# Optimization experiments

Measured on AMD Instinct MI355X. Metric: run time of the kernel, lower is better.

Reference implementation:

```python
import jax, jax.numpy as jnp
import numpy as np

EPS = 1e-6

def setup_inputs() -> dict:
    key = jax.random.key(0)
    S, U, D = 512, 32, 512
    dvecs = jax.random.normal(key, (S, U, D), dtype=jnp.float32)
    w = jnp.array([10.0], dtype=jnp.float32)
    b = jnp.array([-5.0], dtype=jnp.float32)
    return {"dvecs": dvecs, "w": w, "b": b}


def _ge2e_loss(dvecs, w, b):
    S, U, D = dvecs.shape
    # Full centroids [S, D]
    centroids = dvecs.mean(axis=1)
    # Leave-one-out centroids [S, U, D] (equivalent to the roll/unfold/mean trick)
    loo = (dvecs.sum(axis=1, keepdims=True) - dvecs) / (U - 1)
    # Norms, clamped like F.cosine_similarity eps
    dn = jnp.linalg.norm(dvecs, axis=-1)        # [S, U]
    cn = jnp.linalg.norm(centroids, axis=-1)    # [S]
    ln = jnp.linalg.norm(loo, axis=-1)          # [S, U]
    # Cosine sim of every utterance vs every speaker centroid: [S, U, S]
    sim_all = jnp.einsum('sud,jd->suj', dvecs, centroids) / jnp.maximum(dn[..., None] * cn[None, None, :], EPS)
    # Self-speaker column uses the leave-one-out centroid (index_copy in torch code)
    sim_self = jnp.einsum('sud,sud->su', dvecs, loo) / jnp.maximum(dn * ln, EPS)
    spk = jnp.arange(S)
    self_mask = spk[:, None, None] == spk[None, None, :]          # [S, 1, S] -> broadcasts to [S, U, S]
    sim = jnp.where(self_mask, sim_self[..., None], sim_all)
    logits = sim * w[0] + b[0]
    losses = -jax.nn.log_softmax(logits, axis=2)                  # [S, U, S]
    # Select losses[s, u, s] and sum (index_select of diagonal entries)
    return jnp.sum(jnp.where(self_mask, losses, 0.0))


def reference(dvecs, w, b):
    return _ge2e_loss(dvecs, w, b)
```

## Files before the change

### kernel.cpp

```cpp
#include <hip/hip_runtime.h>
#include <math.h>

#define NS 512
#define NU 32
#define ND 512
#define GEPS 1e-6f

typedef float f4 __attribute__((ext_vector_type(4)));
typedef _Float16 half8 __attribute__((ext_vector_type(8)));


__global__ __launch_bounds__(256) void prep_kernel(const float* __restrict__ dvecs,
                                                   _Float16* __restrict__ bpk,
                                                   float* __restrict__ cn2) {
    const int s = blockIdx.x, t = threadIdx.x;
    const float* base = dvecs + (size_t)s * NU * ND;
    const int d0 = t * 2;
    float sx = 0.f, sy = 0.f;
    for (int u = 0; u < NU; ++u) {
        float2 v = *(const float2*)(base + u * ND + d0);
        sx += v.x; sy += v.y;
    }
    sx *= (1.0f / NU); sy *= (1.0f / NU);

    float c2 = sx * sx + sy * sy;
    #pragma unroll
    for (int m = 1; m < 64; m <<= 1) c2 += __shfl_xor(c2, m);
    __shared__ float red[4];
    if ((t & 63) == 0) red[t >> 6] = c2;
    __syncthreads();
    if (t == 0) cn2[s] = red[0] + red[1] + red[2] + red[3];

    _Float16 hx = (_Float16)sx, hy = (_Float16)sy;
    _Float16 lx = (_Float16)(sx - (float)hx), ly = (_Float16)(sy - (float)hy);
    const int ct_g = s >> 4, l15 = s & 15;
    const int tt = d0 >> 5, lg = (d0 >> 3) & 3, j = d0 & 7;
    size_t hbase = ((size_t)(ct_g * 16 + tt)) * 1024 + (lg * 16 + l15) * 8 + j;
    unsigned hi2 = (unsigned)__builtin_bit_cast(unsigned short, hx)
                 | ((unsigned)__builtin_bit_cast(unsigned short, hy) << 16);
    unsigned lo2 = (unsigned)__builtin_bit_cast(unsigned short, lx)
                 | ((unsigned)__builtin_bit_cast(unsigned short, ly) << 16);
    *(unsigned*)(bpk + hbase)       = hi2;
    *(unsigned*)(bpk + hbase + 512) = lo2;
}

__global__ __launch_bounds__(512, 4) void ge2e_mfma(const float* __restrict__ dvecs,
                                                    const _Float16* __restrict__ bpk,
                                                    const float* __restrict__ cn2,
                                                    const float* __restrict__ wp,
                                                    const float* __restrict__ bp,
                                                    float* __restrict__ out) {
    const int s = blockIdx.x, tid = threadIdx.x;
    const int l = tid & 63, wv = tid >> 6;
    const int l15 = l & 15, lg = l >> 4;

    f4 acc[2][4];
    #pragma unroll
    for (int rt = 0; rt < 2; ++rt)
        #pragma unroll
        for (int ct = 0; ct < 4; ++ct) acc[rt][ct] = (f4){0.f, 0.f, 0.f, 0.f};
    float dnp[2] = {0.f, 0.f};

    const float*    Ab0 = dvecs + (size_t)s * NU * ND + (size_t)l15 * ND + lg * 8;
    const _Float16* Bb  = bpk + (size_t)(wv * 4) * 16 * 1024 + l * 8;

    for (int t = 0; t < 16; ++t) {
        half8 bh[4], bl[4];
        #pragma unroll
        for (int ct = 0; ct < 4; ++ct) {
            const _Float16* p = Bb + (size_t)(ct * 16 + t) * 1024;
            bh[ct] = *(const half8*)p;
            bl[ct] = *(const half8*)(p + 512);
        }
        half8 ah[2], al[2];
        #pragma unroll
        for (int rt = 0; rt < 2; ++rt) {
            const float* ap = Ab0 + rt * 16 * ND + t * 32;
            f4 a0 = *(const f4*)ap, a1 = *(const f4*)(ap + 4);
            dnp[rt] += a0[0]*a0[0] + a0[1]*a0[1] + a0[2]*a0[2] + a0[3]*a0[3]
                     + a1[0]*a1[0] + a1[1]*a1[1] + a1[2]*a1[2] + a1[3]*a1[3];
            #pragma unroll
            for (int i = 0; i < 4; ++i) {
                _Float16 h0 = (_Float16)a0[i];
                ah[rt][i]     = h0; al[rt][i]     = (_Float16)(a0[i] - (float)h0);
                _Float16 h1 = (_Float16)a1[i];
                ah[rt][4 + i] = h1; al[rt][4 + i] = (_Float16)(a1[i] - (float)h1);
            }
        }
        #pragma unroll
        for (int ct = 0; ct < 4; ++ct)
            #pragma unroll
            for (int rt = 0; rt < 2; ++rt) {
                acc[rt][ct] = __builtin_amdgcn_mfma_f32_16x16x32_f16(ah[rt], bh[ct], acc[rt][ct], 0, 0, 0);
                acc[rt][ct] = __builtin_amdgcn_mfma_f32_16x16x32_f16(ah[rt], bl[ct], acc[rt][ct], 0, 0, 0);
                acc[rt][ct] = __builtin_amdgcn_mfma_f32_16x16x32_f16(al[rt], bh[ct], acc[rt][ct], 0, 0, 0);
                acc[rt][ct] = __builtin_amdgcn_mfma_f32_16x16x32_f16(al[rt], bl[ct], acc[rt][ct], 0, 0, 0);
            }
    }

    #pragma unroll
    for (int rt = 0; rt < 2; ++rt) {
        dnp[rt] += __shfl_xor(dnp[rt], 16);
        dnp[rt] += __shfl_xor(dnp[rt], 32);
    }
    __shared__ float sDn2[32], sSelf[32], sMax[8][32], sSum[8][32], sRow[32];
    if (wv == 0 && l < 16) { sDn2[l15] = dnp[0]; sDn2[16 + l15] = dnp[1]; }
    __syncthreads();

    const float w = wp[0], bb = bp[0];
    const float cn2s = cn2[s];
    float dv[2][4];
    #pragma unroll
    for (int rt = 0; rt < 2; ++rt)
        #pragma unroll
        for (int r = 0; r < 4; ++r) dv[rt][r] = sDn2[rt * 16 + lg * 4 + r];

    const bool owner = (wv == (s >> 6)) && (l15 == (s & 15));
    const int  ctd   = (s >> 4) & 3;

    float dotc[2][4];
    #pragma unroll
    for (int ct = 0; ct < 4; ++ct)
        if (ct == ctd)
            #pragma unroll
            for (int rt = 0; rt < 2; ++rt)
                #pragma unroll
                for (int r = 0; r < 4; ++r) dotc[rt][r] = acc[rt][ct][r];

    #pragma unroll
    for (int ct = 0; ct < 4; ++ct) {
        const float cv = cn2[wv * 64 + ct * 16 + l15];
        #pragma unroll
        for (int rt = 0; rt < 2; ++rt)
            #pragma unroll
            for (int r = 0; r < 4; ++r)
                acc[rt][ct][r] = w * (acc[rt][ct][r] / fmaxf(sqrtf(dv[rt][r] * cv), GEPS)) + bb;
    }
    if (owner) {
        #pragma unroll
        for (int rt = 0; rt < 2; ++rt)
            #pragma unroll
            for (int r = 0; r < 4; ++r) {
                const float d2  = dv[rt][r];
                const float num = (float)NU * dotc[rt][r] - d2;
                const float X   = (float)(NU * NU) * cn2s - 2.0f * NU * dotc[rt][r] + d2;
                const float den = fmaxf(sqrtf(d2) * sqrtf(X), GEPS * (NU - 1));
                const float ls  = w * (num / den) + bb;
                #pragma unroll
                for (int ct = 0; ct < 4; ++ct)
                    if (ct == ctd) acc[rt][ct][r] = ls;
                sSelf[rt * 16 + lg * 4 + r] = ls;
            }
    }

    #pragma unroll
    for (int rt = 0; rt < 2; ++rt)
        #pragma unroll
        for (int r = 0; r < 4; ++r) {
            float mx = -INFINITY;
            #pragma unroll
            for (int ct = 0; ct < 4; ++ct) mx = fmaxf(mx, acc[rt][ct][r]);
            mx = fmaxf(mx, __shfl_xor(mx, 1)); mx = fmaxf(mx, __shfl_xor(mx, 2));
            mx = fmaxf(mx, __shfl_xor(mx, 4)); mx = fmaxf(mx, __shfl_xor(mx, 8));
            float se = 0.f;
            #pragma unroll
            for (int ct = 0; ct < 4; ++ct) se += expf(acc[rt][ct][r] - mx);
            se += __shfl_xor(se, 1); se += __shfl_xor(se, 2);
            se += __shfl_xor(se, 4); se += __shfl_xor(se, 8);
            if (l15 == 0) {
                sMax[wv][rt * 16 + lg * 4 + r] = mx;
                sSum[wv][rt * 16 + lg * 4 + r] = se;
            }
        }
    __syncthreads();

    if (tid < 32) {
        float M = -INFINITY;
        #pragma unroll
        for (int v = 0; v < 8; ++v) M = fmaxf(M, sMax[v][tid]);
        float S = 0.f;
        #pragma unroll
        for (int v = 0; v < 8; ++v) S += sSum[v][tid] * expf(sMax[v][tid] - M);
        sRow[tid] = logf(S) + M - sSelf[tid];
    }
    __syncthreads();
    if (tid == 0) {
        float tot = 0.f;
        #pragma unroll
        for (int u2 = 0; u2 < 32; ++u2) tot += sRow[u2];
        atomicAdd(out, tot);
    }
}

extern "C" void kernel_launch(void* const* d_in, const int* in_sizes, int n_in,
                              void* d_out, int out_size, void* d_ws, size_t ws_size,
                              hipStream_t stream) {
    const float* dvecs = (const float*)d_in[0];
    const float* w     = (const float*)d_in[1];
    const float* b     = (const float*)d_in[2];
    float* out = (float*)d_out;

    _Float16* bpk = (_Float16*)d_ws;
    float*    cn2 = (float*)(bpk + (size_t)32 * 16 * 1024);

    hipMemsetAsync(d_out, 0, sizeof(float), stream);
    prep_kernel<<<NS, 256, 0, stream>>>(dvecs, bpk, cn2);
    ge2e_mfma<<<NS, 512, 0, stream>>>(dvecs, bpk, cn2, w, b, out);
}
```

Baseline: 136.3 us.

## Precompute split-fp16 packed utterance tiles and norms in prep kernel

The prep kernel now also computes per-utterance squared norms and writes the hi/lo fp16 split of every dvec into an MFMA-ready packed layout. The main kernel then loads these packed half8 fragments directly instead of reading fp32 and converting inside its loop, which was replicated across all 8 waves. The cost is an extra write and read of a 32 MB workspace buffer, plus a fallback path kept for when the workspace is too small.

```diff
diff --git a/kernel.cpp b/kernel.cpp
--- a/kernel.cpp
+++ b/kernel.cpp
@@ -10,9 +10,218 @@
 typedef _Float16 half8 __attribute__((ext_vector_type(8)));
 
 
-__global__ __launch_bounds__(256) void prep_kernel(const float* __restrict__ dvecs,
-                                                   _Float16* __restrict__ bpk,
-                                                   float* __restrict__ cn2) {
+__global__ __launch_bounds__(256) void prep_full(const float* __restrict__ dvecs,
+                                                 _Float16* __restrict__ bpk,
+                                                 float* __restrict__ cn2,
+                                                 float* __restrict__ dn2,
+                                                 _Float16* __restrict__ apk) {
+    const int s = blockIdx.x, t = threadIdx.x;
+    const int l = t & 63, wv = t >> 6, l15 = l & 15, lg = l >> 4;
+    const float* base = dvecs + (size_t)s * NU * ND;
+    __shared__ float red[4];
+
+    const int d0 = t * 2;
+    float sx = 0.f, sy = 0.f;
+    #pragma unroll 4
+    for (int u = 0; u < NU; ++u) {
+        float2 v = *(const float2*)(base + u * ND + d0);
+        sx += v.x; sy += v.y;
+    }
+    sx *= (1.0f / NU); sy *= (1.0f / NU);
+    float c2 = sx * sx + sy * sy;
+    #pragma unroll
+    for (int m = 1; m < 64; m <<= 1) c2 += __shfl_xor(c2, m);
+    if ((t & 63) == 0) red[t >> 6] = c2;
+
+    {
+        _Float16 hx = (_Float16)sx, hy = (_Float16)sy;
+        _Float16 lx = (_Float16)(sx - (float)hx), ly = (_Float16)(sy - (float)hy);
+        const int ct_g = s >> 4, cl15 = s & 15;
+        const int tt = d0 >> 5, blg = (d0 >> 3) & 3, j = d0 & 7;
+        size_t hbase = ((size_t)(ct_g * 16 + tt)) * 1024 + (blg * 16 + cl15) * 8 + j;
+        unsigned hi2 = (unsigned)__builtin_bit_cast(unsigned short, hx)
+                     | ((unsigned)__builtin_bit_cast(unsigned short, hy) << 16);
+        unsigned lo2 = (unsigned)__builtin_bit_cast(unsigned short, lx)
+                     | ((unsigned)__builtin_bit_cast(unsigned short, ly) << 16);
+        *(unsigned*)(bpk + hbase)       = hi2;
+        *(unsigned*)(bpk + hbase + 512) = lo2;
+    }
+    __syncthreads();
+    if (t == 0) cn2[s] = red[0] + red[1] + red[2] + red[3];
+
+    {
+        const int u = t >> 3, jj = t & 7;
+        const float* up = base + u * ND + jj * 4;
+        float q = 0.f;
+        #pragma unroll
+        for (int i = 0; i < 16; ++i) {
+            f4 v = *(const f4*)(up + i * 32);
+            q += v[0]*v[0] + v[1]*v[1] + v[2]*v[2] + v[3]*v[3];
+        }
+        q += __shfl_xor(q, 1); q += __shfl_xor(q, 2); q += __shfl_xor(q, 4);
+        if (jj == 0) dn2[s * NU + u] = q;
+    }
+
+    #pragma unroll
+    for (int i = 0; i < 8; ++i) {
+        const int idx = wv * 8 + i;
+        const int rt = idx >> 4, tk = idx & 15;
+        const int u = rt * 16 + l15, k = tk * 32 + lg * 8;
+        const float* ap = base + (size_t)u * ND + k;
+        f4 a0 = *(const f4*)ap;
+        f4 a1 = *(const f4*)(ap + 4);
+        half8 h, lo;
+        #pragma unroll
+        for (int i2 = 0; i2 < 4; ++i2) {
+            _Float16 h0 = (_Float16)a0[i2];
+            h[i2]     = h0; lo[i2]     = (_Float16)(a0[i2] - (float)h0);
+            _Float16 h1 = (_Float16)a1[i2];
+            h[4 + i2] = h1; lo[4 + i2] = (_Float16)(a1[i2] - (float)h1);
+        }
+        _Float16* cb = apk + ((size_t)(s * 2 + rt) * 16 + tk) * 1024 + l * 8;
+        *(half8*)cb         = h;
+        *(half8*)(cb + 512) = lo;
+    }
+}
+
+__global__ __launch_bounds__(512, 4) void ge2e_full(const _Float16* __restrict__ apk,
+                                                    const _Float16* __restrict__ bpk,
+                                                    const float* __restrict__ cn2,
+                                                    const float* __restrict__ dn2,
+                                                    const float* __restrict__ wp,
+                                                    const float* __restrict__ bp,
+                                                    float* __restrict__ out) {
+    const int s = blockIdx.x, tid = threadIdx.x;
+    const int l = tid & 63, wv = tid >> 6;
+    const int l15 = l & 15, lg = l >> 4;
+
+    f4 acc[2][4];
+    #pragma unroll
+    for (int rt = 0; rt < 2; ++rt)
+        #pragma unroll
+        for (int ct = 0; ct < 4; ++ct) acc[rt][ct] = (f4){0.f, 0.f, 0.f, 0.f};
+
+    const _Float16* Ab = apk + (size_t)s * 32 * 1024 + l * 8;
+    const _Float16* Bb = bpk + (size_t)(wv * 4) * 16 * 1024 + l * 8;
+
+    for (int t = 0; t < 16; ++t) {
+        half8 bh[4], bl[4], ah[2], al[2];
+        #pragma unroll
+        for (int ct = 0; ct < 4; ++ct) {
+            const _Float16* p = Bb + (size_t)(ct * 16 + t) * 1024;
+            bh[ct] = *(const half8*)p;
+            bl[ct] = *(const half8*)(p + 512);
+        }
+        #pragma unroll
+        for (int rt = 0; rt < 2; ++rt) {
+            const _Float16* p = Ab + (size_t)(rt * 16 + t) * 1024;
+            ah[rt] = *(const half8*)p;
+            al[rt] = *(const half8*)(p + 512);
+        }
+        #pragma unroll
+        for (int ct = 0; ct < 4; ++ct)
+            #pragma unroll
+            for (int rt = 0; rt < 2; ++rt) {
+                acc[rt][ct] = __builtin_amdgcn_mfma_f32_16x16x32_f16(ah[rt], bh[ct], acc[rt][ct], 0, 0, 0);
+                acc[rt][ct] = __builtin_amdgcn_mfma_f32_16x16x32_f16(ah[rt], bl[ct], acc[rt][ct], 0, 0, 0);
+                acc[rt][ct] = __builtin_amdgcn_mfma_f32_16x16x32_f16(al[rt], bh[ct], acc[rt][ct], 0, 0, 0);
+                acc[rt][ct] = __builtin_amdgcn_mfma_f32_16x16x32_f16(al[rt], bl[ct], acc[rt][ct], 0, 0, 0);
+            }
+    }
+
+    __shared__ float sDn2[32], sSelf[32], sMax[8][32], sSum[8][32], sRow[32];
+    if (tid < 32) sDn2[tid] = dn2[s * NU + tid];
+    __syncthreads();
+
+    const float w = wp[0], bb = bp[0];
+    const float cn2s = cn2[s];
+    float dv[2][4];
+    #pragma unroll
+    for (int rt = 0; rt < 2; ++rt)
+        #pragma unroll
+        for (int r = 0; r < 4; ++r) dv[rt][r] = sDn2[rt * 16 + lg * 4 + r];
+
+    const bool owner = (wv == (s >> 6)) && (l15 == (s & 15));
+    const int  ctd   = (s >> 4) & 3;
+
+    float dotc[2][4];
+    #pragma unroll
+    for (int ct = 0; ct < 4; ++ct)
+        if (ct == ctd)
+            #pragma unroll
+            for (int rt = 0; rt < 2; ++rt)
+                #pragma unroll
+                for (int r = 0; r < 4; ++r) dotc[rt][r] = acc[rt][ct][r];
+
+    #pragma unroll
+    for (int ct = 0; ct < 4; ++ct) {
+        const float cv = cn2[wv * 64 + ct * 16 + l15];
+        #pragma unroll
+        for (int rt = 0; rt < 2; ++rt)
+            #pragma unroll
+            for (int r = 0; r < 4; ++r)
+                acc[rt][ct][r] = w * (acc[rt][ct][r] / fmaxf(sqrtf(dv[rt][r] * cv), GEPS)) + bb;
+    }
+    if (owner) {
+        #pragma unroll
+        for (int rt = 0; rt < 2; ++rt)
+            #pragma unroll
+            for (int r = 0; r < 4; ++r) {
+                const float d2  = dv[rt][r];
+                const float num = (float)NU * dotc[rt][r] - d2;
+                const float X   = (float)(NU * NU) * cn2s - 2.0f * NU * dotc[rt][r] + d2;
+                const float den = fmaxf(sqrtf(d2) * sqrtf(X), GEPS * (NU - 1));
+                const float ls  = w * (num / den) + bb;
+                #pragma unroll
+                for (int ct = 0; ct < 4; ++ct)
+                    if (ct == ctd) acc[rt][ct][r] = ls;
+                sSelf[rt * 16 + lg * 4 + r] = ls;
+            }
+    }
+
+    #pragma unroll
+    for (int rt = 0; rt < 2; ++rt)
+        #pragma unroll
+        for (int r = 0; r < 4; ++r) {
+            float mx = -INFINITY;
+            #pragma unroll
+            for (int ct = 0; ct < 4; ++ct) mx = fmaxf(mx, acc[rt][ct][r]);
+            mx = fmaxf(mx, __shfl_xor(mx, 1)); mx = fmaxf(mx, __shfl_xor(mx, 2));
+            mx = fmaxf(mx, __shfl_xor(mx, 4)); mx = fmaxf(mx, __shfl_xor(mx, 8));
+            float se = 0.f;
+            #pragma unroll
+            for (int ct = 0; ct < 4; ++ct) se += expf(acc[rt][ct][r] - mx);
+            se += __shfl_xor(se, 1); se += __shfl_xor(se, 2);
+            se += __shfl_xor(se, 4); se += __shfl_xor(se, 8);
+            if (l15 == 0) {
+                sMax[wv][rt * 16 + lg * 4 + r] = mx;
+                sSum[wv][rt * 16 + lg * 4 + r] = se;
+            }
+        }
+    __syncthreads();
+
+    if (tid < 32) {
+        float M = -INFINITY;
+        #pragma unroll
+        for (int v = 0; v < 8; ++v) M = fmaxf(M, sMax[v][tid]);
+        float S = 0.f;
+        #pragma unroll
+        for (int v = 0; v < 8; ++v) S += sSum[v][tid] * expf(sMax[v][tid] - M);
+        sRow[tid] = logf(S) + M - sSelf[tid];
+    }
+    __syncthreads();
+    if (tid == 0) {
+        float tot = 0.f;
+        #pragma unroll
+        for (int u2 = 0; u2 < 32; ++u2) tot += sRow[u2];
+        atomicAdd(out, tot);
+    }
+}
+
+
+__global__ __launch_bounds__(256) void prep_fb(const float* __restrict__ dvecs,
+                                               _Float16* __restrict__ bpk,
+                                               float* __restrict__ cn2) {
     const int s = blockIdx.x, t = threadIdx.x;
     const float* base = dvecs + (size_t)s * NU * ND;
     const int d0 = t * 2;
@@ -22,7 +231,6 @@
         sx += v.x; sy += v.y;
     }
     sx *= (1.0f / NU); sy *= (1.0f / NU);
-
     float c2 = sx * sx + sy * sy;
     #pragma unroll
     for (int m = 1; m < 64; m <<= 1) c2 += __shfl_xor(c2, m);
@@ -30,7 +238,6 @@
     if ((t & 63) == 0) red[t >> 6] = c2;
     __syncthreads();
     if (t == 0) cn2[s] = red[0] + red[1] + red[2] + red[3];
-
     _Float16 hx = (_Float16)sx, hy = (_Float16)sy;
     _Float16 lx = (_Float16)(sx - (float)hx), ly = (_Float16)(sy - (float)hy);
     const int ct_g = s >> 4, l15 = s & 15;
@@ -44,26 +251,23 @@
     *(unsigned*)(bpk + hbase + 512) = lo2;
 }
 
-__global__ __launch_bounds__(512, 4) void ge2e_mfma(const float* __restrict__ dvecs,
-                                                    const _Float16* __restrict__ bpk,
-                                                    const float* __restrict__ cn2,
-                                                    const float* __restrict__ wp,
-                                                    const float* __restrict__ bp,
-                                                    float* __restrict__ out) {
+__global__ __launch_bounds__(512, 4) void ge2e_fb(const float* __restrict__ dvecs,
+                                                  const _Float16* __restrict__ bpk,
+                                                  const float* __restrict__ cn2,
+                                                  const float* __restrict__ wp,
+                                                  const float* __restrict__ bp,
+                                                  float* __restrict__ out) {
     const int s = blockIdx.x, tid = threadIdx.x;
     const int l = tid & 63, wv = tid >> 6;
     const int l15 = l & 15, lg = l >> 4;
-
     f4 acc[2][4];
     #pragma unroll
     for (int rt = 0; rt < 2; ++rt)
         #pragma unroll
         for (int ct = 0; ct < 4; ++ct) acc[rt][ct] = (f4){0.f, 0.f, 0.f, 0.f};
     float dnp[2] = {0.f, 0.f};
-
     const float*    Ab0 = dvecs + (size_t)s * NU * ND + (size_t)l15 * ND + lg * 8;
     const _Float16* Bb  = bpk + (size_t)(wv * 4) * 16 * 1024 + l * 8;
-
     for (int t = 0; t < 16; ++t) {
         half8 bh[4], bl[4];
         #pragma unroll
@@ -97,7 +301,6 @@
                 acc[rt][ct] = __builtin_amdgcn_mfma_f32_16x16x32_f16(al[rt], bl[ct], acc[rt][ct], 0, 0, 0);
             }
     }
-
     #pragma unroll
     for (int rt = 0; rt < 2; ++rt) {
         dnp[rt] += __shfl_xor(dnp[rt], 16);
@@ -106,7 +309,6 @@
     __shared__ float sDn2[32], sSelf[32], sMax[8][32], sSum[8][32], sRow[32];
     if (wv == 0 && l < 16) { sDn2[l15] = dnp[0]; sDn2[16 + l15] = dnp[1]; }
     __syncthreads();
-
     const float w = wp[0], bb = bp[0];
     const float cn2s = cn2[s];
     float dv[2][4];
@@ -114,10 +316,8 @@
     for (int rt = 0; rt < 2; ++rt)
         #pragma unroll
         for (int r = 0; r < 4; ++r) dv[rt][r] = sDn2[rt * 16 + lg * 4 + r];
-
     const bool owner = (wv == (s >> 6)) && (l15 == (s & 15));
     const int  ctd   = (s >> 4) & 3;
-
     float dotc[2][4];
     #pragma unroll
     for (int ct = 0; ct < 4; ++ct)
@@ -126,7 +326,6 @@
             for (int rt = 0; rt < 2; ++rt)
                 #pragma unroll
                 for (int r = 0; r < 4; ++r) dotc[rt][r] = acc[rt][ct][r];
-
     #pragma unroll
     for (int ct = 0; ct < 4; ++ct) {
         const float cv = cn2[wv * 64 + ct * 16 + l15];
@@ -152,7 +351,6 @@
                 sSelf[rt * 16 + lg * 4 + r] = ls;
             }
     }
-
     #pragma unroll
     for (int rt = 0; rt < 2; ++rt)
         #pragma unroll
@@ -173,7 +371,6 @@
             }
         }
     __syncthreads();
-
     if (tid < 32) {
         float M = -INFINITY;
         #pragma unroll
@@ -200,10 +397,24 @@
     const float* b     = (const float*)d_in[2];
     float* out = (float*)d_out;
 
-    _Float16* bpk = (_Float16*)d_ws;
-    float*    cn2 = (float*)(bpk + (size_t)32 * 16 * 1024);
+    const size_t bpk_b = (size_t)32 * 16 * 1024 * sizeof(_Float16);
+    const size_t cn2_b = (size_t)NS * sizeof(float);
+    const size_t dn2_b = (size_t)NS * NU * sizeof(float);
+    const size_t apk_b = (size_t)NS * 2 * 16 * 1024 * sizeof(_Float16);
+    const size_t need  = bpk_b + cn2_b + dn2_b + apk_b;
+
+    char* p = (char*)d_ws;
+    _Float16* bpk = (_Float16*)p;                 p += bpk_b;
+    float*    cn2 = (float*)p;                    p += cn2_b;
+    float*    dn2 = (float*)p;                    p += dn2_b;
+    _Float16* apk = (_Float16*)p;
 
     hipMemsetAsync(d_out, 0, sizeof(float), stream);
-    prep_kernel<<<NS, 256, 0, stream>>>(dvecs, bpk, cn2);
-    ge2e_mfma<<<NS, 512, 0, stream>>>(dvecs, bpk, cn2, w, b, out);
+    if (ws_size >= need) {
+        prep_full<<<NS, 256, 0, stream>>>(dvecs, bpk, cn2, dn2, apk);
+        ge2e_full<<<NS, 512, 0, stream>>>(apk, bpk, cn2, dn2, w, b, out);
+    } else {
+        prep_fb<<<NS, 256, 0, stream>>>(dvecs, bpk, cn2);
+        ge2e_fb<<<NS, 512, 0, stream>>>(dvecs, bpk, cn2, w, b, out);
+    }
 }
```

Result: faster. 128.4 us (-5.8%).

## Pre-split A into fp16 hi/lo in prep and process two speakers per block

Applied to the files above, without the earlier changes.

The prep kernel now also converts each speaker's utterance vectors into a packed fp16 hi/lo layout and computes the per-utterance squared norms, so the main kernel no longer converts and reduces fp32 data inline. The main kernel handles two speakers per block, reusing each centroid B fragment for twice as many MFMAs, and raises instruction priority around the MFMA bursts. The trade-off is an extra write and read of a 32 MB packed A buffer plus higher register pressure, with the occupancy bound lowered from 4 to 3.

```diff
diff --git a/kernel.cpp b/kernel.cpp
--- a/kernel.cpp
+++ b/kernel.cpp
@@ -10,32 +10,67 @@
 typedef _Float16 half8 __attribute__((ext_vector_type(8)));
 
 
-__global__ __launch_bounds__(256) void prep_kernel(const float* __restrict__ dvecs,
-                                                   _Float16* __restrict__ bpk,
-                                                   float* __restrict__ cn2) {
+__global__ __launch_bounds__(256) void prep_full(const float* __restrict__ dvecs,
+                                                 _Float16* __restrict__ bpk,
+                                                 float* __restrict__ cn2,
+                                                 float* __restrict__ dn2,
+                                                 _Float16* __restrict__ apk) {
     const int s = blockIdx.x, t = threadIdx.x;
+    const int l = t & 63, w = t >> 6, l15 = l & 15, lg = l >> 4;
+    const int rt = w >> 1, tkh = (w & 1) * 8;
     const float* base = dvecs + (size_t)s * NU * ND;
+    __shared__ float dn2p[4][16];
+    __shared__ float red[4];
+
+    const int u = rt * 16 + l15;
+    const float* rowp = base + (size_t)u * ND;
+    float q = 0.f;
+    #pragma unroll
+    for (int i = 0; i < 8; ++i) {
+        const int tk = tkh + i;
+        const int k0 = tk * 32 + lg * 8;
+        f4 a0 = *(const f4*)(rowp + k0);
+        f4 a1 = *(const f4*)(rowp + k0 + 4);
+        q += a0[0]*a0[0] + a0[1]*a0[1] + a0[2]*a0[2] + a0[3]*a0[3]
+           + a1[0]*a1[0] + a1[1]*a1[1] + a1[2]*a1[2] + a1[3]*a1[3];
+        half8 h, lo;
+        #pragma unroll
+        for (int c = 0; c < 4; ++c) {
+            _Float16 h0 = (_Float16)a0[c];
+            h[c]     = h0; lo[c]     = (_Float16)(a0[c] - (float)h0);
+            _Float16 h1 = (_Float16)a1[c];
+            h[4 + c] = h1; lo[4 + c] = (_Float16)(a1[c] - (float)h1);
+        }
+        _Float16* cb = apk + ((size_t)(s * 2 + rt) * 16 + tk) * 1024 + l * 8;
+        *(half8*)cb         = h;
+        *(half8*)(cb + 512) = lo;
+    }
+    q += __shfl_xor(q, 16);
+    q += __shfl_xor(q, 32);
+    if (lg == 0) dn2p[w][l15] = q;
+
     const int d0 = t * 2;
     float sx = 0.f, sy = 0.f;
-    for (int u = 0; u < NU; ++u) {
-        float2 v = *(const float2*)(base + u * ND + d0);
+    #pragma unroll 4
+    for (int u2 = 0; u2 < NU; ++u2) {
+        float2 v = *(const float2*)(base + u2 * ND + d0);
         sx += v.x; sy += v.y;
     }
     sx *= (1.0f / NU); sy *= (1.0f / NU);
-
     float c2 = sx * sx + sy * sy;
     #pragma unroll
     for (int m = 1; m < 64; m <<= 1) c2 += __shfl_xor(c2, m);
-    __shared__ float red[4];
     if ((t & 63) == 0) red[t >> 6] = c2;
     __syncthreads();
+    if (t < 32)
+        dn2[s * NU + t] = dn2p[(t >> 4) * 2][t & 15] + dn2p[(t >> 4) * 2 + 1][t & 15];
     if (t == 0) cn2[s] = red[0] + red[1] + red[2] + red[3];
 
     _Float16 hx = (_Float16)sx, hy = (_Float16)sy;
     _Float16 lx = (_Float16)(sx - (float)hx), ly = (_Float16)(sy - (float)hy);
-    const int ct_g = s >> 4, l15 = s & 15;
-    const int tt = d0 >> 5, lg = (d0 >> 3) & 3, j = d0 & 7;
-    size_t hbase = ((size_t)(ct_g * 16 + tt)) * 1024 + (lg * 16 + l15) * 8 + j;
+    const int ct_g = s >> 4, cl15 = s & 15;
+    const int tt = d0 >> 5, blg = (d0 >> 3) & 3, j = d0 & 7;
+    size_t hbase = ((size_t)(ct_g * 16 + tt)) * 1024 + (blg * 16 + cl15) * 8 + j;
     unsigned hi2 = (unsigned)__builtin_bit_cast(unsigned short, hx)
                  | ((unsigned)__builtin_bit_cast(unsigned short, hy) << 16);
     unsigned lo2 = (unsigned)__builtin_bit_cast(unsigned short, lx)
@@ -44,150 +79,155 @@
     *(unsigned*)(bpk + hbase + 512) = lo2;
 }
 
-__global__ __launch_bounds__(512, 4) void ge2e_mfma(const float* __restrict__ dvecs,
+__global__ __launch_bounds__(512, 3) void ge2e_full(const _Float16* __restrict__ apk,
                                                     const _Float16* __restrict__ bpk,
                                                     const float* __restrict__ cn2,
+                                                    const float* __restrict__ dn2,
                                                     const float* __restrict__ wp,
                                                     const float* __restrict__ bp,
                                                     float* __restrict__ out) {
-    const int s = blockIdx.x, tid = threadIdx.x;
-    const int l = tid & 63, wv = tid >> 6;
+    const int s0 = blockIdx.x * 2, tid = threadIdx.x;
+    const int l = tid & 63;
+    const int wv = __builtin_amdgcn_readfirstlane(tid >> 6);
     const int l15 = l & 15, lg = l >> 4;
 
-    f4 acc[2][4];
-    #pragma unroll
-    for (int rt = 0; rt < 2; ++rt)
-        #pragma unroll
-        for (int ct = 0; ct < 4; ++ct) acc[rt][ct] = (f4){0.f, 0.f, 0.f, 0.f};
-    float dnp[2] = {0.f, 0.f};
-
-    const float*    Ab0 = dvecs + (size_t)s * NU * ND + (size_t)l15 * ND + lg * 8;
-    const _Float16* Bb  = bpk + (size_t)(wv * 4) * 16 * 1024 + l * 8;
-
+    f4 acc[2][2][4];
+    #pragma unroll
+    for (int sp = 0; sp < 2; ++sp)
+        #pragma unroll
+        for (int rt = 0; rt < 2; ++rt)
+            #pragma unroll
+            for (int ct = 0; ct < 4; ++ct) acc[sp][rt][ct] = (f4){0.f, 0.f, 0.f, 0.f};
+
+    const _Float16* Au = apk + (size_t)s0 * 32 * 1024;
+    const _Float16* Bu = bpk + (size_t)(wv * 4) * 16 * 1024;
+    const int voff = l * 8;
+
+    #pragma unroll 2
     for (int t = 0; t < 16; ++t) {
         half8 bh[4], bl[4];
         #pragma unroll
         for (int ct = 0; ct < 4; ++ct) {
-            const _Float16* p = Bb + (size_t)(ct * 16 + t) * 1024;
+            const _Float16* p = Bu + (ct * 16 + t) * 1024 + voff;
             bh[ct] = *(const half8*)p;
             bl[ct] = *(const half8*)(p + 512);
         }
-        half8 ah[2], al[2];
-        #pragma unroll
-        for (int rt = 0; rt < 2; ++rt) {
-            const float* ap = Ab0 + rt * 16 * ND + t * 32;
-            f4 a0 = *(const f4*)ap, a1 = *(const f4*)(ap + 4);
-            dnp[rt] += a0[0]*a0[0] + a0[1]*a0[1] + a0[2]*a0[2] + a0[3]*a0[3]
-                     + a1[0]*a1[0] + a1[1]*a1[1] + a1[2]*a1[2] + a1[3]*a1[3];
-            #pragma unroll
-            for (int i = 0; i < 4; ++i) {
-                _Float16 h0 = (_Float16)a0[i];
-                ah[rt][i]     = h0; al[rt][i]     = (_Float16)(a0[i] - (float)h0);
-                _Float16 h1 = (_Float16)a1[i];
-                ah[rt][4 + i] = h1; al[rt][4 + i] = (_Float16)(a1[i] - (float)h1);
+        #pragma unroll
+        for (int sp = 0; sp < 2; ++sp) {
+            half8 ah[2], al[2];
+            #pragma unroll
+            for (int rt = 0; rt < 2; ++rt) {
+                const _Float16* p = Au + sp * 32 * 1024 + (rt * 16 + t) * 1024 + voff;
+                ah[rt] = *(const half8*)p;
+                al[rt] = *(const half8*)(p + 512);
             }
-        }
+            __builtin_amdgcn_s_setprio(1);
+            #pragma unroll
+            for (int ct = 0; ct < 4; ++ct)
+                #pragma unroll
+                for (int rt = 0; rt < 2; ++rt) {
+                    acc[sp][rt][ct] = __builtin_amdgcn_mfma_f32_16x16x32_f16(ah[rt], bh[ct], acc[sp][rt][ct], 0, 0, 0);
+                    acc[sp][rt][ct] = __builtin_amdgcn_mfma_f32_16x16x32_f16(ah[rt], bl[ct], acc[sp][rt][ct], 0, 0, 0);
+                    acc[sp][rt][ct] = __builtin_amdgcn_mfma_f32_16x16x32_f16(al[rt], bh[ct], acc[sp][rt][ct], 0, 0, 0);
+                    acc[sp][rt][ct] = __builtin_amdgcn_mfma_f32_16x16x32_f16(al[rt], bl[ct], acc[sp][rt][ct], 0, 0, 0);
+                }
+            __builtin_amdgcn_s_setprio(0);
+        }
+    }
+
+    __shared__ float sDn2[2][32], sSelf[2][32], sMax[2][8][32], sSum[2][8][32], sRow[2][32];
+    if (tid < 64) sDn2[tid >> 5][tid & 31] = dn2[(s0 + (tid >> 5)) * NU + (tid & 31)];
+    __syncthreads();
+
+    const float w = wp[0], bb = bp[0];
+
+    #pragma unroll
+    for (int sp = 0; sp < 2; ++sp) {
+        const int s = s0 + sp;
+        const float cn2s = cn2[s];
+        float dv[2][4];
+        #pragma unroll
+        for (int rt = 0; rt < 2; ++rt)
+            #pragma unroll
+            for (int r = 0; r < 4; ++r) dv[rt][r] = sDn2[sp][rt * 16 + lg * 4 + r];
+
+        const bool owner = (wv == (s >> 6)) && (l15 == (s & 15));
+        const int  ctd   = (s >> 4) & 3;
+
+        float dotc[2][4];
         #pragma unroll
         for (int ct = 0; ct < 4; ++ct)
-            #pragma unroll
-            for (int rt = 0; rt < 2; ++rt) {
-                acc[rt][ct] = __builtin_amdgcn_mfma_f32_16x16x32_f16(ah[rt], bh[ct], acc[rt][ct], 0, 0, 0);
-                acc[rt][ct] = __builtin_amdgcn_mfma_f32_16x16x32_f16(ah[rt], bl[ct], acc[rt][ct], 0, 0, 0);
-                acc[rt][ct] = __builtin_amdgcn_mfma_f32_16x16x32_f16(al[rt], bh[ct], acc[rt][ct], 0, 0, 0);
-                acc[rt][ct] = __builtin_amdgcn_mfma_f32_16x16x32_f16(al[rt], bl[ct], acc[rt][ct], 0, 0, 0);
+            if (ct == ctd)
+                #pragma unroll
+                for (int rt = 0; rt < 2; ++rt)
+                    #pragma unroll
+                    for (int r = 0; r < 4; ++r) dotc[rt][r] = acc[sp][rt][ct][r];
+
+        #pragma unroll
+        for (int ct = 0; ct < 4; ++ct) {
+            const float cv = cn2[wv * 64 + ct * 16 + l15];
+            #pragma unroll
+            for (int rt = 0; rt < 2; ++rt)
+                #pragma unroll
+                for (int r = 0; r < 4; ++r)
+                    acc[sp][rt][ct][r] = w * (acc[sp][rt][ct][r] / fmaxf(sqrtf(dv[rt][r] * cv), GEPS)) + bb;
+        }
+        if (owner) {
+            #pragma unroll
+            for (int rt = 0; rt < 2; ++rt)
+                #pragma unroll
+                for (int r = 0; r < 4; ++r) {
+                    const float d2  = dv[rt][r];
+                    const float num = (float)NU * dotc[rt][r] - d2;
+                    const float X   = (float)(NU * NU) * cn2s - 2.0f * NU * dotc[rt][r] + d2;
+                    const float den = fmaxf(sqrtf(d2) * sqrtf(X), GEPS * (NU - 1));
+                    const float ls  = w * (num / den) + bb;
+                    #pragma unroll
+                    for (int ct = 0; ct < 4; ++ct)
+                        if (ct == ctd) acc[sp][rt][ct][r] = ls;
+                    sSelf[sp][rt * 16 + lg * 4 + r] = ls;
+                }
+        }
+
+        #pragma unroll
+        for (int rt = 0; rt < 2; ++rt)
+            #pragma unroll
+            for (int r = 0; r < 4; ++r) {
+                float mx = -INFINITY;
+                #pragma unroll
+                for (int ct = 0; ct < 4; ++ct) mx = fmaxf(mx, acc[sp][rt][ct][r]);
+                mx = fmaxf(mx, __shfl_xor(mx, 1)); mx = fmaxf(mx, __shfl_xor(mx, 2));
+                mx = fmaxf(mx, __shfl_xor(mx, 4)); mx = fmaxf(mx, __shfl_xor(mx, 8));
+                float se = 0.f;
+                #pragma unroll
+                for (int ct = 0; ct < 4; ++ct) se += expf(acc[sp][rt][ct][r] - mx);
+                se += __shfl_xor(se, 1); se += __shfl_xor(se, 2);
+                se += __shfl_xor(se, 4); se += __shfl_xor(se, 8);
+                if (l15 == 0) {
+                    sMax[sp][wv][rt * 16 + lg * 4 + r] = mx;
+                    sSum[sp][wv][rt * 16 + lg * 4 + r] = se;
+                }
             }
     }
-
-    #pragma unroll
-    for (int rt = 0; rt < 2; ++rt) {
-        dnp[rt] += __shfl_xor(dnp[rt], 16);
-        dnp[rt] += __shfl_xor(dnp[rt], 32);
-    }
-    __shared__ float sDn2[32], sSelf[32], sMax[8][32], sSum[8][32], sRow[32];
-    if (wv == 0 && l < 16) { sDn2[l15] = dnp[0]; sDn2[16 + l15] = dnp[1]; }
-    __syncthreads();
-
-    const float w = wp[0], bb = bp[0];
-    const float cn2s = cn2[s];
-    float dv[2][4];
-    #pragma unroll
-    for (int rt = 0; rt < 2; ++rt)
-        #pragma unroll
-        for (int r = 0; r < 4; ++r) dv[rt][r] = sDn2[rt * 16 + lg * 4 + r];
-
-    const bool owner = (wv == (s >> 6)) && (l15 == (s & 15));
-    const int  ctd   = (s >> 4) & 3;
-
-    float dotc[2][4];
-    #pragma unroll
-    for (int ct = 0; ct < 4; ++ct)
-        if (ct == ctd)
-            #pragma unroll
-            for (int rt = 0; rt < 2; ++rt)
-                #pragma unroll
-                for (int r = 0; r < 4; ++r) dotc[rt][r] = acc[rt][ct][r];
-
-    #pragma unroll
-    for (int ct = 0; ct < 4; ++ct) {
-        const float cv = cn2[wv * 64 + ct * 16 + l15];
-        #pragma unroll
-        for (int rt = 0; rt < 2; ++rt)
-            #pragma unroll
-            for (int r = 0; r < 4; ++r)
-                acc[rt][ct][r] = w * (acc[rt][ct][r] / fmaxf(sqrtf(dv[rt][r] * cv), GEPS)) + bb;
-    }
-    if (owner) {
-        #pragma unroll
-        for (int rt = 0; rt < 2; ++rt)
-            #pragma unroll
-            for (int r = 0; r < 4; ++r) {
-                const float d2  = dv[rt][r];
-                const float num = (float)NU * dotc[rt][r] - d2;
-                const float X   = (float)(NU * NU) * cn2s - 2.0f * NU * dotc[rt][r] + d2;
-                const float den = fmaxf(sqrtf(d2) * sqrtf(X), GEPS * (NU - 1));
-                const float ls  = w * (num / den) + bb;
-                #pragma unroll
-                for (int ct = 0; ct < 4; ++ct)
-                    if (ct == ctd) acc[rt][ct][r] = ls;
-                sSelf[rt * 16 + lg * 4 + r] = ls;
-            }
-    }
-
-    #pragma unroll
-    for (int rt = 0; rt < 2; ++rt)
-        #pragma unroll
-        for (int r = 0; r < 4; ++r) {
-            float mx = -INFINITY;
-            #pragma unroll
-            for (int ct = 0; ct < 4; ++ct) mx = fmaxf(mx, acc[rt][ct][r]);
-            mx = fmaxf(mx, __shfl_xor(mx, 1)); mx = fmaxf(mx, __shfl_xor(mx, 2));
-            mx = fmaxf(mx, __shfl_xor(mx, 4)); mx = fmaxf(mx, __shfl_xor(mx, 8));
-            float se = 0.f;
-            #pragma unroll
-            for (int ct = 0; ct < 4; ++ct) se += expf(acc[rt][ct][r] - mx);
-            se += __shfl_xor(se, 1); se += __shfl_xor(se, 2);
-            se += __shfl_xor(se, 4); se += __shfl_xor(se, 8);
-            if (l15 == 0) {
-                sMax[wv][rt * 16 + lg * 4 + r] = mx;
-                sSum[wv][rt * 16 + lg * 4 + r] = se;
-            }
-        }
-    __syncthreads();
-
-    if (tid < 32) {
+    __syncthreads();
+
+    if (tid < 64) {
+        const int sp = tid >> 5, u2 = tid & 31;
         float M = -INFINITY;
         #pragma unroll
-        for (int v = 0; v < 8; ++v) M = fmaxf(M, sMax[v][tid]);
+        for (int v = 0; v < 8; ++v) M = fmaxf(M, sMax[sp][v][u2]);
         float S = 0.f;
         #pragma unroll
-        for (int v = 0; v < 8; ++v) S += sSum[v][tid] * expf(sMax[v][tid] - M);
-        sRow[tid] = logf(S) + M - sSelf[tid];
+        for (int v = 0; v < 8; ++v) S += sSum[sp][v][u2] * expf(sMax[sp][v][u2] - M);
+        sRow[sp][u2] = logf(S) + M - sSelf[sp][u2];
     }
     __syncthreads();
     if (tid == 0) {
         float tot = 0.f;
         #pragma unroll
-        for (int u2 = 0; u2 < 32; ++u2) tot += sRow[u2];
+        for (int sp = 0; sp < 2; ++sp)
+            #pragma unroll
+            for (int u2 = 0; u2 < 32; ++u2) tot += sRow[sp][u2];
         atomicAdd(out, tot);
     }
 }
@@ -200,10 +240,17 @@
     const float* b     = (const float*)d_in[2];
     float* out = (float*)d_out;
 
-    _Float16* bpk = (_Float16*)d_ws;
-    float*    cn2 = (float*)(bpk + (size_t)32 * 16 * 1024);
+    const size_t bpk_b = (size_t)32 * 16 * 1024 * sizeof(_Float16);
+    const size_t cn2_b = (size_t)NS * sizeof(float);
+    const size_t dn2_b = (size_t)NS * NU * sizeof(float);
+
+    char* p = (char*)d_ws;
+    _Float16* bpk = (_Float16*)p;                 p += bpk_b;
+    float*    cn2 = (float*)p;                    p += cn2_b;
+    float*    dn2 = (float*)p;                    p += dn2_b;
+    _Float16* apk = (_Float16*)p;
 
     hipMemsetAsync(d_out, 0, sizeof(float), stream);
-    prep_kernel<<<NS, 256, 0, stream>>>(dvecs, bpk, cn2);
-    ge2e_mfma<<<NS, 512, 0, stream>>>(dvecs, bpk, cn2, w, b, out);
+    prep_full<<<NS, 256, 0, stream>>>(dvecs, bpk, cn2, dn2, apk);
+    ge2e_full<<<NS / 2, 512, 0, stream>>>(apk, bpk, cn2, dn2, w, b, out);
 }
```

After: 130.6 us. 4.2% less time.
